# Performance work log

Hardware: AMD Instinct MI355X
Metric: run time of the kernel (lower is better)

Reference implementation:

```python
import jax, jax.numpy as jnp
import numpy as np

N_NODES = 100000
N_FEAT = 128
HID = 8
HEADS1 = 8
OUT2 = 32
NEG_SLOPE = 0.2


def gat_conv(x, W, a_src, a_dst, b, src, dst, n_nodes, concat):
    # x: [N, Fin], W: [Fin, H*C], a_src/a_dst: [H, C], b: [H*C] or [C]
    H, C = a_src.shape
    h = (x @ W).reshape(n_nodes, H, C)                      # [N, H, C]
    e_src = jnp.sum(h * a_src, axis=-1)                     # [N, H]
    e_dst = jnp.sum(h * a_dst, axis=-1)                     # [N, H]
    e = jax.nn.leaky_relu(e_src[src] + e_dst[dst], NEG_SLOPE)  # [E, H]
    m = jax.ops.segment_max(e, dst, num_segments=n_nodes)   # [N, H] (self-loops => no empty segment)
    ex = jnp.exp(e - m[dst])                                # [E, H]
    denom = jax.ops.segment_sum(ex, dst, num_segments=n_nodes)
    alpha = ex / denom[dst]                                 # [E, H]
    out = jax.ops.segment_sum(alpha[:, :, None] * h[src], dst, num_segments=n_nodes)  # [N, H, C]
    out = out.reshape(n_nodes, H * C) if concat else out.mean(axis=1)
    return out + b


def setup_inputs() -> dict:
    key = jax.random.key(0)
    ks = jax.random.split(key, 12)
    x = jax.random.normal(ks[0], (N_NODES, N_FEAT), dtype=jnp.float32)
    edge_index = jax.random.randint(ks[1], (2, 3200000), 0, N_NODES, dtype=jnp.int64)
    s1 = 1.0 / np.sqrt(N_FEAT)
    s2 = 1.0 / np.sqrt(HID * HEADS1)
    return {
        "x": x,
        "edge_index": edge_index,
        "W1": jax.random.normal(ks[2], (N_FEAT, HEADS1 * HID), dtype=jnp.float32) * s1,
        "a_src1": jax.random.normal(ks[3], (HEADS1, HID), dtype=jnp.float32) * s2,
        "a_dst1": jax.random.normal(ks[4], (HEADS1, HID), dtype=jnp.float32) * s2,
        "b1": jnp.zeros((HEADS1 * HID,), dtype=jnp.float32),
        "W2": jax.random.normal(ks[5], (HEADS1 * HID, OUT2), dtype=jnp.float32) * s2,
        "a_src2": jax.random.normal(ks[6], (1, OUT2), dtype=jnp.float32) * (1.0 / np.sqrt(OUT2)),
        "a_dst2": jax.random.normal(ks[7], (1, OUT2), dtype=jnp.float32) * (1.0 / np.sqrt(OUT2)),
        "b2": jnp.zeros((OUT2,), dtype=jnp.float32),
        "Wr": jax.random.normal(ks[8], (OUT2, 1), dtype=jnp.float32) * (1.0 / np.sqrt(OUT2)),
        "br": jnp.zeros((1,), dtype=jnp.float32),
    }


def reference(x, edge_index, W1, a_src1, a_dst1, b1, W2, a_src2, a_dst2, b2, Wr, br):
    n = x.shape[0]
    # PyG GATConv default add_self_loops=True
    loops = jnp.arange(n, dtype=edge_index.dtype)
    src = jnp.concatenate([edge_index[0], loops])
    dst = jnp.concatenate([edge_index[1], loops])
    h = gat_conv(x, W1, a_src1, a_dst1, b1, src, dst, n, concat=True)   # [N, 64]
    h = jax.nn.elu(h)
    h = gat_conv(h, W2, a_src2, a_dst2, b2, src, dst, n, concat=False)  # [N, 32]
    pooled = jnp.sum(h, axis=0, keepdims=True)                          # SumAggregation -> [1, 32]
    return pooled @ Wr + br                                             # [1, 1]
```

## Files before the change

### kernel.cpp

```cpp
#include <hip/hip_runtime.h>
#include <math.h>

#define NEG_SLOPE 0.2f
#define FIN 128
#define H1 8
#define F1 64
#define F2 32

#define SHIFT 5
#define BW 32
#define CAPL 2048
#define CAP_G 1408
#define NBMAX 4096

#define SB_SHIFT 11
#define NSBMAX 64
#define P_CHUNK 2048
#define BPS 35
#define SBCAP (BPS * P_CHUNK)

typedef unsigned short ushort_t;
typedef unsigned int uint_t;

#define LO16(u) __uint_as_float((u) << 16)
#define HI16(u) __uint_as_float((u) & 0xffff0000u)

#define FOLDQ4(x) { x += __shfl_xor(x, 16, 64); x += __shfl_xor(x, 32, 64); }
#define FOLD64(x) { x += __shfl_xor(x, 1, 64); x += __shfl_xor(x, 2, 64); x += __shfl_xor(x, 4, 64); \
                    x += __shfl_xor(x, 8, 64); x += __shfl_xor(x, 16, 64); x += __shfl_xor(x, 32, 64); }

static __device__ __forceinline__ ushort_t f2bf(float f) {
    uint_t u = __float_as_uint(f);
    u = (u + 0x7FFFu + ((u >> 16) & 1u)) >> 16;
    return (ushort_t)u;
}
static __device__ __forceinline__ uint_t packAB(float e) {
    return (uint_t)f2bf(__expf(e)) | ((uint_t)f2bf(__expf(NEG_SLOPE * e)) << 16);
}

__global__ void gemm1_kernel(const float* __restrict__ x, const float* __restrict__ W1,
                             const float* __restrict__ a_src, const float* __restrict__ a_dst,
                             ushort_t* __restrict__ h1, uint_t* __restrict__ sp,
                             float* __restrict__ ed, int N) {
    __shared__ float xs[16][FIN];
    int tid = threadIdx.x;
    int n0 = blockIdx.x * 16;
    for (int i = tid; i < 16 * FIN; i += 256) {
        int nn = n0 + (i >> 7);
        xs[i >> 7][i & 127] = (nn < N) ? x[(size_t)nn * FIN + (i & 127)] : 0.f;
    }
    __syncthreads();
    int wv = tid >> 6, j = tid & 63;
    int nb = wv << 2;
    float a0 = 0.f, a1 = 0.f, a2 = 0.f, a3 = 0.f;
#pragma unroll 2
    for (int k = 0; k < FIN; k += 4) {
        float w0 = W1[(k + 0) * F1 + j];
        float w1 = W1[(k + 1) * F1 + j];
        float w2 = W1[(k + 2) * F1 + j];
        float w3 = W1[(k + 3) * F1 + j];
        float4 x0 = *(const float4*)&xs[nb + 0][k];
        float4 x1 = *(const float4*)&xs[nb + 1][k];
        float4 x2 = *(const float4*)&xs[nb + 2][k];
        float4 x3 = *(const float4*)&xs[nb + 3][k];
        a0 = fmaf(x0.x, w0, fmaf(x0.y, w1, fmaf(x0.z, w2, fmaf(x0.w, w3, a0))));
        a1 = fmaf(x1.x, w0, fmaf(x1.y, w1, fmaf(x1.z, w2, fmaf(x1.w, w3, a1))));
        a2 = fmaf(x2.x, w0, fmaf(x2.y, w1, fmaf(x2.z, w2, fmaf(x2.w, w3, a2))));
        a3 = fmaf(x3.x, w0, fmaf(x3.y, w1, fmaf(x3.z, w2, fmaf(x3.w, w3, a3))));
    }
    float as = a_src[j], ad = a_dst[j];
    float av[4] = {a0, a1, a2, a3};
#pragma unroll
    for (int t = 0; t < 4; ++t) {
        int n = n0 + nb + t;
        if (n >= N) break;
        h1[(size_t)n * F1 + j] = f2bf(av[t]);
        float vs = av[t] * as;
        float vd = av[t] * ad;
#pragma unroll
        for (int off = 4; off >= 1; off >>= 1) {
            vs += __shfl_down(vs, off, 8);
            vd += __shfl_down(vd, off, 8);
        }
        if ((j & 7) == 0) {
            sp[n * H1 + (j >> 3)] = packAB(vs);
            ed[n * H1 + (j >> 3)] = vd;
        }
    }
}

__global__ void zerob_kernel(int* __restrict__ bcnt, int* __restrict__ boff,
                             int NB, float* __restrict__ pooled, int capg,
                             int* __restrict__ sbcnt, int nsb) {
    int t = blockIdx.x * blockDim.x + threadIdx.x;
    int stride = gridDim.x * blockDim.x;
    for (int i = t; i < NB; i += stride) {
        bcnt[i] = 0;
        if (capg) boff[i] = i * capg;
    }
    for (int i = t; i < nsb; i += stride) sbcnt[i] = 0;
    if (t == 0) pooled[0] = 0.f;
}

__global__ void __launch_bounds__(256, 4)
part1_kernel(const int* __restrict__ ei, int E, int N,
             int* __restrict__ sbcnt, uint_t* __restrict__ sbdata) {
    __shared__ int hist[NSBMAX];
    __shared__ int loff[NSBMAX];
    __shared__ int lcur[NSBMAX];
    __shared__ int gb[NSBMAX];
    __shared__ uint_t buf[P_CHUNK];
    __shared__ unsigned char sbarr[P_CHUNK];
    int tid = threadIdx.x;
    int NSB = (N + ((1 << SB_SHIFT) - 1)) >> SB_SHIFT;
    for (int i = tid; i < NSB; i += 256) hist[i] = 0;
    __syncthreads();
    int EN = E + N;
    int base = blockIdx.x * P_CHUNK;
    int m = EN - base; if (m > P_CHUNK) m = P_CHUNK;
    int t0 = base + tid * 8;
    int s[8], d[8];
    bool fast = (t0 + 8 <= E) && ((E & 3) == 0);
    if (fast) {
        int4 a = *(const int4*)&ei[t0];
        int4 b = *(const int4*)&ei[t0 + 4];
        s[0]=a.x; s[1]=a.y; s[2]=a.z; s[3]=a.w; s[4]=b.x; s[5]=b.y; s[6]=b.z; s[7]=b.w;
        int4 c = *(const int4*)&ei[E + t0];
        int4 e2 = *(const int4*)&ei[E + t0 + 4];
        d[0]=c.x; d[1]=c.y; d[2]=c.z; d[3]=c.w; d[4]=e2.x; d[5]=e2.y; d[6]=e2.z; d[7]=e2.w;
    } else {
#pragma unroll
        for (int r = 0; r < 8; ++r) {
            int t = t0 + r;
            if (t < EN) {
                if (t < E) { s[r] = ei[t]; d[r] = ei[E + t]; }
                else       { s[r] = d[r] = t - E; }
            } else d[r] = -1;
        }
    }
#pragma unroll
    for (int r = 0; r < 8; ++r)
        if (d[r] >= 0) atomicAdd(&hist[d[r] >> SB_SHIFT], 1);
    __syncthreads();
    if (tid < 64) {
        int v = (tid < NSB) ? hist[tid] : 0;
        int e = v;
#pragma unroll
        for (int o = 1; o < 64; o <<= 1) {
            int u = __shfl_up(e, o, 64);
            if (tid >= o) e += u;
        }
        e -= v;
        if (tid < NSB) {
            loff[tid] = e;
            lcur[tid] = e;
            gb[tid] = v ? atomicAdd(&sbcnt[tid], v) : 0;
        }
    }
    __syncthreads();
#pragma unroll
    for (int r = 0; r < 8; ++r)
        if (d[r] >= 0) {
            int sb = d[r] >> SB_SHIFT;
            int pos = atomicAdd(&lcur[sb], 1);
            buf[pos] = ((uint_t)s[r] << SB_SHIFT) | (uint_t)(d[r] & ((1 << SB_SHIFT) - 1));
            sbarr[pos] = (unsigned char)sb;
        }
    __syncthreads();
    for (int i = tid; i < m; i += 256) {
        int sb = sbarr[i];
        int idx = gb[sb] + (i - loff[sb]);
        if (idx < SBCAP)
            sbdata[(size_t)sb * SBCAP + idx] = buf[i];
    }
}

__global__ void __launch_bounds__(256, 4)
part2_kernel(const uint_t* __restrict__ sbdata, const int* __restrict__ sbcnt,
             int* __restrict__ bcnt, const int* __restrict__ boff,
             uint_t* __restrict__ pk) {
    __shared__ int hist[64];
    __shared__ int loff[64];
    __shared__ int lcur[64];
    __shared__ int gb[64];
    __shared__ uint_t buf[P_CHUNK];
    int tid = threadIdx.x;
    int sb = blockIdx.x / BPS;
    int base = (blockIdx.x % BPS) * P_CHUNK;
    int cnt = sbcnt[sb];
    if (cnt > SBCAP) cnt = SBCAP;
    if (base >= cnt) return;
    int m = cnt - base; if (m > P_CHUNK) m = P_CHUNK;
    if (tid < 64) hist[tid] = 0;
    __syncthreads();
    const uint_t* src = sbdata + (size_t)sb * SBCAP + base;
    uint_t v[8];
#pragma unroll
    for (int r = 0; r < 8; ++r) {
        int i = tid + r * 256;
        if (i < m) {
            v[r] = src[i];
            atomicAdd(&hist[(v[r] >> 5) & 63], 1);
        }
    }
    __syncthreads();
    if (tid < 64) {
        int c = hist[tid];
        int e = c;
#pragma unroll
        for (int o = 1; o < 64; o <<= 1) {
            int u = __shfl_up(e, o, 64);
            if (tid >= o) e += u;
        }
        e -= c;
        loff[tid] = e;
        lcur[tid] = e;
        int bucket = (sb << 6) + tid;
        gb[tid] = c ? (boff[bucket] + atomicAdd(&bcnt[bucket], c)) : 0;
    }
    __syncthreads();
#pragma unroll
    for (int r = 0; r < 8; ++r) {
        int i = tid + r * 256;
        if (i < m) {
            int lb = (v[r] >> 5) & 63;
            int pos = atomicAdd(&lcur[lb], 1);
            buf[pos] = v[r];
        }
    }
    __syncthreads();
    for (int i = tid; i < m; i += 256) {
        uint_t u = buf[i];
        int lb = (u >> 5) & 63;
        int idx = gb[lb] + (i - loff[lb]);
        pk[idx] = ((u >> SB_SHIFT) << SHIFT) | (u & (BW - 1));
    }
}

__global__ void bhist_kernel(const int* __restrict__ ei, int E, int N,
                             int* __restrict__ bcnt, int NB) {
    __shared__ int h[NBMAX];
    int tid = threadIdx.x;
    for (int i = tid; i < NB; i += 256) h[i] = 0;
    __syncthreads();
    int EN = E + N;
    int chunk = (EN + gridDim.x - 1) / gridDim.x;
    int e0 = blockIdx.x * chunk;
    int e1 = e0 + chunk; if (e1 > EN) e1 = EN;
    for (int t = e0 + tid; t < e1; t += 256) {
        int d = (t < E) ? ei[E + t] : (t - E);
        atomicAdd(&h[d >> SHIFT], 1);
    }
    __syncthreads();
    for (int i = tid; i < NB; i += 256)
        if (h[i]) atomicAdd(&bcnt[i], h[i]);
}

__global__ void bscan_kernel(const int* __restrict__ bcnt, int NB,
                             int* __restrict__ boff, int* __restrict__ bcur) {
    int lane = threadIdx.x;
    int chunk = (NB + 63) >> 6;
    int lo = lane * chunk;
    int hi = lo + chunk; if (hi > NB) hi = NB;
    int sum = 0;
    for (int i = lo; i < hi; ++i) sum += bcnt[i];
    int e = sum;
#pragma unroll
    for (int o = 1; o < 64; o <<= 1) {
        int v = __shfl_up(e, o, 64);
        if (lane >= o) e += v;
    }
    e -= sum;
    int run = e;
    for (int i = lo; i < hi; ++i) {
        int c = bcnt[i];
        boff[i] = run;
        bcur[i] = run;
        run += c;
    }
}

__global__ void bscat_kernel(const int* __restrict__ ei, int E, int N,
                             int* __restrict__ bcur, uint_t* __restrict__ pk, int NB) {
    __shared__ int lh[NBMAX];
    __shared__ int lc[NBMAX];
    int tid = threadIdx.x;
    for (int i = tid; i < NB; i += 256) lh[i] = 0;
    __syncthreads();
    int EN = E + N;
    int chunk = (EN + gridDim.x - 1) / gridDim.x;
    int e0 = blockIdx.x * chunk;
    int e1 = e0 + chunk; if (e1 > EN) e1 = EN;
    for (int t = e0 + tid; t < e1; t += 256) {
        int d = (t < E) ? ei[E + t] : (t - E);
        atomicAdd(&lh[d >> SHIFT], 1);
    }
    __syncthreads();
    for (int i = tid; i < NB; i += 256) {
        int c = lh[i];
        lc[i] = c ? atomicAdd(&bcur[i], c) : 0;
    }
    __syncthreads();
    for (int t = e0 + tid; t < e1; t += 256) {
        int s, d;
        if (t < E) { s = ei[t]; d = ei[E + t]; } else { s = d = t - E; }
        int pos = atomicAdd(&lc[d >> SHIFT], 1);
        pk[pos] = ((uint_t)s << SHIFT) | (uint_t)(d & (BW - 1));
    }
}

__global__ void __launch_bounds__(256, 8)
edge1_fused(const int* __restrict__ bcnt, const int* __restrict__ boff,
            uint_t* __restrict__ pk,
            const uint_t* __restrict__ sp, const float* __restrict__ ed,
            const ushort_t* __restrict__ h1,
            const float* __restrict__ b1, const float* __restrict__ W2,
            const float* __restrict__ a_src2, const float* __restrict__ a_dst2,
            const float* __restrict__ Wr,
            uint2* __restrict__ rec, float* __restrict__ ed2,
            int* __restrict__ loffg, int* __restrict__ ldegg, int N) {
    int b = blockIdx.x;
    int d0 = b << SHIFT;
    int cnt = bcnt[b];
    int gbase = boff[b];
    int tid = threadIdx.x;
    int wv = tid >> 6;
    int L = tid & 63;
    int q = L >> 4;
    int c4 = (L & 15) << 2;
    int hL = (L & 15) >> 1;
    __shared__ int ldeg[BW], loff[BW], lcur[BW];
    __shared__ int lsrc[CAPL];
    __shared__ float a1s[BW][F1];
    if (cnt <= CAPL) {
        if (tid < BW) ldeg[tid] = 0;
        __syncthreads();
        for (int k = tid; k < cnt; k += 256) atomicAdd(&ldeg[pk[gbase + k] & (BW - 1)], 1);
        __syncthreads();
        if (tid < BW) {
            int v = ldeg[tid];
            int e = v;
#pragma unroll
            for (int o = 1; o < BW; o <<= 1) {
                int u = __shfl_up(e, o, 64);
                if (tid >= o) e += u;
            }
            e -= v;
            loff[tid] = e;
            lcur[tid] = e;
        }
        __syncthreads();
        for (int k = tid; k < cnt; k += 256) {
            uint_t v = pk[gbase + k];
            int pos = atomicAdd(&lcur[v & (BW - 1)], 1);
            lsrc[pos] = (int)(v >> SHIFT);
        }
        __syncthreads();
        for (int k = tid; k < cnt; k += 256) pk[gbase + k] = (uint_t)lsrc[k];
        if (tid < BW) {
            loffg[d0 + tid] = loff[tid];
            ldegg[d0 + tid] = ldeg[tid];
        }
        for (int ld = wv * 8; ld < wv * 8 + 8; ++ld) {
            int d = d0 + ld;
            if (d >= N) break;
            int st = loff[ld], en = st + ldeg[ld];
            float edv = ed[d * H1 + hL];
            float Ad = __expf(edv), Bd = __expf(NEG_SLOPE * edv);
            float ax = 0.f, ay = 0.f, az = 0.f, aw = 0.f, wsum = 0.f;
            uint_t U0, U1; uint2 V0, V1;
            {
                int i0 = st + q, i1 = st + 4 + q;
                bool ok0 = i0 < en, ok1 = i1 < en;
                int s0 = lsrc[ok0 ? i0 : st];
                int s1 = lsrc[ok1 ? i1 : st];
                uint_t u0 = sp[s0 * H1 + hL];
                uint_t u1 = sp[s1 * H1 + hL];
                V0 = *(const uint2*)(h1 + ((size_t)s0 << 6) + c4);
                V1 = *(const uint2*)(h1 + ((size_t)s1 << 6) + c4);
                U0 = ok0 ? u0 : 0u;
                U1 = ok1 ? u1 : 0u;
            }
            for (int k = st; k < en; k += 8) {
                uint_t N0, N1; uint2 P0, P1;
                {
                    int i0 = k + 8 + q, i1 = k + 12 + q;
                    bool ok0 = i0 < en, ok1 = i1 < en;
                    int s0 = lsrc[ok0 ? i0 : st];
                    int s1 = lsrc[ok1 ? i1 : st];
                    uint_t u0 = sp[s0 * H1 + hL];
                    uint_t u1 = sp[s1 * H1 + hL];
                    P0 = *(const uint2*)(h1 + ((size_t)s0 << 6) + c4);
                    P1 = *(const uint2*)(h1 + ((size_t)s1 << 6) + c4);
                    N0 = ok0 ? u0 : 0u;
                    N1 = ok1 ? u1 : 0u;
                }
                float w0 = fmaxf(LO16(U0) * Ad, HI16(U0) * Bd);
                float w1 = fmaxf(LO16(U1) * Ad, HI16(U1) * Bd);
                ax = fmaf(w0, LO16(V0.x), ax);
                ay = fmaf(w0, HI16(V0.x), ay);
                az = fmaf(w0, LO16(V0.y), az);
                aw = fmaf(w0, HI16(V0.y), aw);
                ax = fmaf(w1, LO16(V1.x), ax);
                ay = fmaf(w1, HI16(V1.x), ay);
                az = fmaf(w1, LO16(V1.y), az);
                aw = fmaf(w1, HI16(V1.y), aw);
                wsum += w0 + w1;
                U0 = N0; U1 = N1; V0 = P0; V1 = P1;
            }
            FOLDQ4(ax); FOLDQ4(ay); FOLDQ4(az); FOLDQ4(aw); FOLDQ4(wsum);
            if (q == 0) {
                float inv = 1.f / wsum;
                a1s[ld][c4 + 0] = ax * inv;
                a1s[ld][c4 + 1] = ay * inv;
                a1s[ld][c4 + 2] = az * inv;
                a1s[ld][c4 + 3] = aw * inv;
            }
        }
    } else {
        for (int ld = wv * 8; ld < wv * 8 + 8; ++ld) {
            int d = d0 + ld;
            if (d >= N) break;
            float edv = ed[d * H1 + hL];
            float Ad = __expf(edv), Bd = __expf(NEG_SLOPE * edv);
            float ax = 0.f, ay = 0.f, az = 0.f, aw = 0.f, wsum = 0.f;
            for (int k0 = 0; k0 < cnt; k0 += 4) {
                int idx = k0 + q;
                bool ok = idx < cnt;
                uint_t v = pk[gbase + (ok ? idx : 0)];
                int s = (int)(v >> SHIFT);
                bool m = ok && ((int)(v & (BW - 1)) == ld);
                uint_t u = sp[(uint_t)s * H1 + hL];
                float w = m ? fmaxf(LO16(u) * Ad, HI16(u) * Bd) : 0.f;
                uint2 hv = *(const uint2*)(h1 + ((size_t)s << 6) + c4);
                ax = fmaf(w, LO16(hv.x), ax);
                ay = fmaf(w, HI16(hv.x), ay);
                az = fmaf(w, LO16(hv.y), az);
                aw = fmaf(w, HI16(hv.y), aw);
                wsum += w;
            }
            FOLDQ4(ax); FOLDQ4(ay); FOLDQ4(az); FOLDQ4(aw); FOLDQ4(wsum);
            if (q == 0) {
                float inv = 1.f / wsum;
                a1s[ld][c4 + 0] = ax * inv;
                a1s[ld][c4 + 1] = ay * inv;
                a1s[ld][c4 + 2] = az * inv;
                a1s[ld][c4 + 3] = aw * inv;
            }
        }
    }
    int nd = N - d0; if (nd > BW) nd = BW;
    __syncthreads();
    for (int i = tid; i < BW * F1; i += 256) {
        int dd = i >> 6;
        if (dd < nd) {
            int k = i & 63;
            float v = a1s[dd][k] + b1[k];
            a1s[dd][k] = v > 0.f ? v : expm1f(v);
        }
    }
    __syncthreads();
    int half = tid >> 5, j = tid & 31;
#pragma unroll
    for (int pass = 0; pass < 4; ++pass) {
        int ld2 = half + (pass << 3);
        if (ld2 < nd) {
            float acc = 0.f;
#pragma unroll
            for (int k = 0; k < F1; ++k) acc = fmaf(a1s[ld2][k], W2[k * F2 + j], acc);
            float vs = acc * a_src2[j];
            float vd = acc * a_dst2[j];
            float vg = acc * Wr[j];
#pragma unroll
            for (int off = 16; off >= 1; off >>= 1) {
                vs += __shfl_down(vs, off, 32);
                vd += __shfl_down(vd, off, 32);
                vg += __shfl_down(vg, off, 32);
            }
            if (j == 0) {
                int d = d0 + ld2;
                uint2 r; r.x = packAB(vs); r.y = __float_as_uint(vg);
                rec[d] = r;
                ed2[d] = vd;
            }
        }
    }
}

__global__ void __launch_bounds__(256, 8)
edge2_gather(const int* __restrict__ bcnt, const int* __restrict__ boff,
             const uint_t* __restrict__ pk,
             const int* __restrict__ loffg, const int* __restrict__ ldegg,
             const uint2* __restrict__ rec, const float* __restrict__ ed2,
             const float* __restrict__ b2, const float* __restrict__ Wr,
             float* __restrict__ pooled, int N) {
    int b = blockIdx.x;
    int d0 = b << SHIFT;
    int cnt = bcnt[b];
    int gbase = boff[b];
    int tid = threadIdx.x;
    int wv = tid >> 6;
    int L = tid & 63;
    __shared__ float ls[4];
    float t0 = (L < F2) ? b2[L] * Wr[L] : 0.f;
    FOLD64(t0);
    float b2w = t0;
    float part = 0.f;
    if (cnt <= CAPL) {
        for (int ld = wv * 8; ld < wv * 8 + 8; ++ld) {
            int d = d0 + ld;
            if (d >= N) break;
            int st = gbase + loffg[d];
            int dg = ldegg[d];
            float edv = ed2[d];
            float Ad = __expf(edv), Bd = __expf(NEG_SLOPE * edv);
            float acc = 0.f, wsm = 0.f;
            for (int k = 0; k < dg; k += 64) {
                int i = k + L;
                bool ok = i < dg;
                int s = (int)pk[st + (ok ? i : 0)];
                uint2 r = rec[s];
                float w = ok ? fmaxf(LO16(r.x) * Ad, HI16(r.x) * Bd) : 0.f;
                acc = fmaf(w, __uint_as_float(r.y), acc);
                wsm += w;
            }
            FOLD64(acc); FOLD64(wsm);
            part += acc / wsm + b2w;
        }
    } else {
        for (int ld = wv * 8; ld < wv * 8 + 8; ++ld) {
            int d = d0 + ld;
            if (d >= N) break;
            float edv = ed2[d];
            float Ad = __expf(edv), Bd = __expf(NEG_SLOPE * edv);
            float acc = 0.f, wsm = 0.f;
            for (int k0 = 0; k0 < cnt; k0 += 64) {
                int i = k0 + L;
                bool ok = i < cnt;
                uint_t v = pk[gbase + (ok ? i : 0)];
                int s = (int)(v >> SHIFT);
                bool mm = ok && ((int)(v & (BW - 1)) == ld);
                uint2 r = rec[s];
                float w = mm ? fmaxf(LO16(r.x) * Ad, HI16(r.x) * Bd) : 0.f;
                acc = fmaf(w, __uint_as_float(r.y), acc);
                wsm += w;
            }
            FOLD64(acc); FOLD64(wsm);
            part += acc / wsm + b2w;
        }
    }
    if (L == 0) ls[wv] = part;
    __syncthreads();
    if (tid == 0) atomicAdd(pooled, ls[0] + ls[1] + ls[2] + ls[3]);
}

__global__ void final_kernel(const float* __restrict__ pooled, const float* __restrict__ br,
                             float* __restrict__ out) {
    if (threadIdx.x == 0 && blockIdx.x == 0) out[0] = pooled[0] + br[0];
}

static inline size_t al128(size_t v) { return (v + 127) & ~(size_t)127; }

extern "C" void kernel_launch(void* const* d_in, const int* in_sizes, int n_in,
                              void* d_out, int out_size, void* d_ws, size_t ws_size,
                              hipStream_t stream) {
    const float* x    = (const float*)d_in[0];
    const int*   ei   = (const int*)d_in[1];
    const float* W1   = (const float*)d_in[2];
    const float* a_s1 = (const float*)d_in[3];
    const float* a_d1 = (const float*)d_in[4];
    const float* b1   = (const float*)d_in[5];
    const float* W2   = (const float*)d_in[6];
    const float* a_s2 = (const float*)d_in[7];
    const float* a_d2 = (const float*)d_in[8];
    const float* b2   = (const float*)d_in[9];
    const float* Wr   = (const float*)d_in[10];
    const float* br   = (const float*)d_in[11];
    float* out = (float*)d_out;

    int N = in_sizes[0] / FIN;
    int E = in_sizes[1] / 2;
    size_t n = (size_t)N;
    int NB = (N + BW - 1) >> SHIFT;
    int NSB = (N + ((1 << SB_SHIFT) - 1)) >> SB_SHIFT;

    char* ws = (char*)d_ws;
    size_t off_scr = 0;
    size_t off_sp1 = al128(off_scr + n * 256);
    size_t off_ed1 = al128(off_sp1 + n * 32 + 32);
    size_t off_h1  = al128(off_ed1 + n * 32);
    size_t off_pk  = al128(off_h1 + n * 128 + 128);
    uint_t*   sp1  = (uint_t*)(ws + off_sp1);
    float*    ed1  = (float*)(ws + off_ed1);
    ushort_t* h1   = (ushort_t*)(ws + off_h1);
    uint_t*   pk   = (uint_t*)(ws + off_pk);
    size_t pk_static = (size_t)NB * CAP_G * 4;
    size_t pk_exact  = (size_t)(E + N) * 4;
    uint_t* sbdata = (uint_t*)(ws + off_scr);
    size_t off_rec  = off_scr;
    size_t off_ed2  = al128(off_rec + (size_t)NB * BW * 8);
    size_t off_lofg = al128(off_ed2 + (size_t)NB * BW * 4);
    size_t off_ldgg = al128(off_lofg + (size_t)NB * BW * 4);
    uint2* rec   = (uint2*)(ws + off_rec);
    float* ed2   = (float*)(ws + off_ed2);
    int*   loffg = (int*)(ws + off_lofg);
    int*   ldegg = (int*)(ws + off_ldgg);
    bool use_static = (NSB <= NSBMAX) &&
                      ((size_t)NSB * SBCAP * 4 <= n * 256) &&
                      (off_ldgg + (size_t)NB * BW * 4 <= n * 256) &&
                      (ws_size >= off_pk + pk_static + (size_t)NBMAX * 16 +
                                  (size_t)NSBMAX * 4 + 128);
    char* tail = ws + off_pk + (use_static ? pk_static : pk_exact);
    int*      bcnt  = (int*)tail;
    int*      boff  = (int*)(tail + NBMAX * 4);
    int*      bcur  = (int*)(tail + NBMAX * 8);
    int*      sbcnt = (int*)(tail + NBMAX * 12);
    float*  pooled  = (float*)(tail + NBMAX * 12 + NSBMAX * 4);

    zerob_kernel<<<8, 256, 0, stream>>>(bcnt, boff, NB, pooled,
                                        use_static ? CAP_G : 0, sbcnt, NSB);
    if (use_static) {
        int EN = E + N;
        int G1 = (EN + P_CHUNK - 1) / P_CHUNK;
        part1_kernel<<<G1, 256, 0, stream>>>(ei, E, N, sbcnt, sbdata);
        part2_kernel<<<NSB * BPS, 256, 0, stream>>>(sbdata, sbcnt, bcnt, boff, pk);
        gemm1_kernel<<<(N + 15) / 16, 256, 0, stream>>>(x, W1, a_s1, a_d1, h1, sp1, ed1, N);
    } else {
        gemm1_kernel<<<(N + 15) / 16, 256, 0, stream>>>(x, W1, a_s1, a_d1, h1, sp1, ed1, N);
        bhist_kernel<<<256, 256, 0, stream>>>(ei, E, N, bcnt, NB);
        bscan_kernel<<<1, 64, 0, stream>>>(bcnt, NB, boff, bcur);
        bscat_kernel<<<256, 256, 0, stream>>>(ei, E, N, bcur, pk, NB);
    }
    edge1_fused<<<NB, 256, 0, stream>>>(bcnt, boff, pk, sp1, ed1, h1,
                                        b1, W2, a_s2, a_d2, Wr,
                                        rec, ed2, loffg, ldegg, N);
    edge2_gather<<<NB, 256, 0, stream>>>(bcnt, boff, pk, loffg, ldegg,
                                         rec, ed2, b2, Wr, pooled, N);
    final_kernel<<<1, 64, 0, stream>>>(pooled, br, out);
}
```

Baseline: 372.7 us.

## Use per-wavefront LDS histograms and vectorize the layer-2 projection

Shared-memory histogram and cursor counters in the two partition kernels and the layer-1 gather are split into four per-wavefront copies. Their offsets are derived from the combined prefix scan, which is meant to cut LDS atomic contention on hot buckets. The per-node 64x32 projection at the end of the layer-1 kernel is remapped so each thread computes 4 outputs with float4 loads from a padded shared array and then reduces across 8 lanes. This replaces the old scheme of 32 lanes each doing a full scalar dot product. The changes add LDS footprint and a slightly more complex scan, and the per-wave cursors change the order of edges within a bucket.

```diff
diff --git a/kernel.cpp b/kernel.cpp
--- a/kernel.cpp
+++ b/kernel.cpp
@@ -5,6 +5,7 @@
 #define FIN 128
 #define H1 8
 #define F1 64
+#define F1P 68
 #define F2 32
 
 #define SHIFT 5
@@ -105,15 +106,16 @@
 __global__ void __launch_bounds__(256, 4)
 part1_kernel(const int* __restrict__ ei, int E, int N,
              int* __restrict__ sbcnt, uint_t* __restrict__ sbdata) {
-    __shared__ int hist[NSBMAX];
+    __shared__ int histw[4][NSBMAX];
+    __shared__ int lcurw[4][NSBMAX];
     __shared__ int loff[NSBMAX];
-    __shared__ int lcur[NSBMAX];
     __shared__ int gb[NSBMAX];
     __shared__ uint_t buf[P_CHUNK];
     __shared__ unsigned char sbarr[P_CHUNK];
     int tid = threadIdx.x;
+    int wv = tid >> 6;
     int NSB = (N + ((1 << SB_SHIFT) - 1)) >> SB_SHIFT;
-    for (int i = tid; i < NSB; i += 256) hist[i] = 0;
+    for (int i = tid; i < 4 * NSBMAX; i += 256) ((int*)histw)[i] = 0;
     __syncthreads();
     int EN = E + N;
     int base = blockIdx.x * P_CHUNK;
@@ -140,21 +142,29 @@
     }
 #pragma unroll
     for (int r = 0; r < 8; ++r)
-        if (d[r] >= 0) atomicAdd(&hist[d[r] >> SB_SHIFT], 1);
+        if (d[r] >= 0) atomicAdd(&histw[wv][d[r] >> SB_SHIFT], 1);
     __syncthreads();
     if (tid < 64) {
-        int v = (tid < NSB) ? hist[tid] : 0;
-        int e = v;
+        int h0 = 0, h1 = 0, h2 = 0, h3 = 0;
+        if (tid < NSB) {
+            h0 = histw[0][tid]; h1 = histw[1][tid];
+            h2 = histw[2][tid]; h3 = histw[3][tid];
+        }
+        int tot = h0 + h1 + h2 + h3;
+        int e = tot;
 #pragma unroll
         for (int o = 1; o < 64; o <<= 1) {
             int u = __shfl_up(e, o, 64);
             if (tid >= o) e += u;
         }
-        e -= v;
+        e -= tot;
         if (tid < NSB) {
             loff[tid] = e;
-            lcur[tid] = e;
-            gb[tid] = v ? atomicAdd(&sbcnt[tid], v) : 0;
+            gb[tid] = tot ? atomicAdd(&sbcnt[tid], tot) : 0;
+            lcurw[0][tid] = e;
+            lcurw[1][tid] = e + h0;
+            lcurw[2][tid] = e + h0 + h1;
+            lcurw[3][tid] = e + h0 + h1 + h2;
         }
     }
     __syncthreads();
@@ -162,7 +172,7 @@
     for (int r = 0; r < 8; ++r)
         if (d[r] >= 0) {
             int sb = d[r] >> SB_SHIFT;
-            int pos = atomicAdd(&lcur[sb], 1);
+            int pos = atomicAdd(&lcurw[wv][sb], 1);
             buf[pos] = ((uint_t)s[r] << SB_SHIFT) | (uint_t)(d[r] & ((1 << SB_SHIFT) - 1));
             sbarr[pos] = (unsigned char)sb;
         }
@@ -179,19 +189,20 @@
 part2_kernel(const uint_t* __restrict__ sbdata, const int* __restrict__ sbcnt,
              int* __restrict__ bcnt, const int* __restrict__ boff,
              uint_t* __restrict__ pk) {
-    __shared__ int hist[64];
+    __shared__ int histw[4][64];
+    __shared__ int lcurw[4][64];
     __shared__ int loff[64];
-    __shared__ int lcur[64];
     __shared__ int gb[64];
     __shared__ uint_t buf[P_CHUNK];
     int tid = threadIdx.x;
+    int wv = tid >> 6;
     int sb = blockIdx.x / BPS;
     int base = (blockIdx.x % BPS) * P_CHUNK;
     int cnt = sbcnt[sb];
     if (cnt > SBCAP) cnt = SBCAP;
     if (base >= cnt) return;
     int m = cnt - base; if (m > P_CHUNK) m = P_CHUNK;
-    if (tid < 64) hist[tid] = 0;
+    for (int i = tid; i < 4 * 64; i += 256) ((int*)histw)[i] = 0;
     __syncthreads();
     const uint_t* src = sbdata + (size_t)sb * SBCAP + base;
     uint_t v[8];
@@ -200,23 +211,28 @@
         int i = tid + r * 256;
         if (i < m) {
             v[r] = src[i];
-            atomicAdd(&hist[(v[r] >> 5) & 63], 1);
+            atomicAdd(&histw[wv][(v[r] >> 5) & 63], 1);
         }
     }
     __syncthreads();
     if (tid < 64) {
-        int c = hist[tid];
-        int e = c;
+        int h0 = histw[0][tid], h1 = histw[1][tid];
+        int h2 = histw[2][tid], h3 = histw[3][tid];
+        int tot = h0 + h1 + h2 + h3;
+        int e = tot;
 #pragma unroll
         for (int o = 1; o < 64; o <<= 1) {
             int u = __shfl_up(e, o, 64);
             if (tid >= o) e += u;
         }
-        e -= c;
+        e -= tot;
         loff[tid] = e;
-        lcur[tid] = e;
         int bucket = (sb << 6) + tid;
-        gb[tid] = c ? (boff[bucket] + atomicAdd(&bcnt[bucket], c)) : 0;
+        gb[tid] = tot ? (boff[bucket] + atomicAdd(&bcnt[bucket], tot)) : 0;
+        lcurw[0][tid] = e;
+        lcurw[1][tid] = e + h0;
+        lcurw[2][tid] = e + h0 + h1;
+        lcurw[3][tid] = e + h0 + h1 + h2;
     }
     __syncthreads();
 #pragma unroll
@@ -224,7 +240,7 @@
         int i = tid + r * 256;
         if (i < m) {
             int lb = (v[r] >> 5) & 63;
-            int pos = atomicAdd(&lcur[lb], 1);
+            int pos = atomicAdd(&lcurw[wv][lb], 1);
             buf[pos] = v[r];
         }
     }
@@ -329,16 +345,20 @@
     int q = L >> 4;
     int c4 = (L & 15) << 2;
     int hL = (L & 15) >> 1;
-    __shared__ int ldeg[BW], loff[BW], lcur[BW];
+    __shared__ int ldeg[BW], loff[BW];
+    __shared__ int ldegw[4][BW], lcurw[4][BW];
     __shared__ int lsrc[CAPL];
-    __shared__ float a1s[BW][F1];
+    __shared__ float a1s[BW][F1P];
     if (cnt <= CAPL) {
-        if (tid < BW) ldeg[tid] = 0;
+        for (int i = tid; i < 4 * BW; i += 256) ((int*)ldegw)[i] = 0;
         __syncthreads();
-        for (int k = tid; k < cnt; k += 256) atomicAdd(&ldeg[pk[gbase + k] & (BW - 1)], 1);
+        for (int k = tid; k < cnt; k += 256)
+            atomicAdd(&ldegw[wv][pk[gbase + k] & (BW - 1)], 1);
         __syncthreads();
         if (tid < BW) {
-            int v = ldeg[tid];
+            int h0 = ldegw[0][tid], h1_ = ldegw[1][tid];
+            int h2 = ldegw[2][tid], h3 = ldegw[3][tid];
+            int v = h0 + h1_ + h2 + h3;
             int e = v;
 #pragma unroll
             for (int o = 1; o < BW; o <<= 1) {
@@ -347,12 +367,16 @@
             }
             e -= v;
             loff[tid] = e;
-            lcur[tid] = e;
+            ldeg[tid] = v;
+            lcurw[0][tid] = e;
+            lcurw[1][tid] = e + h0;
+            lcurw[2][tid] = e + h0 + h1_;
+            lcurw[3][tid] = e + h0 + h1_ + h2;
         }
         __syncthreads();
         for (int k = tid; k < cnt; k += 256) {
             uint_t v = pk[gbase + k];
-            int pos = atomicAdd(&lcur[v & (BW - 1)], 1);
+            int pos = atomicAdd(&lcurw[wv][v & (BW - 1)], 1);
             lsrc[pos] = (int)(v >> SHIFT);
         }
         __syncthreads();
@@ -460,29 +484,39 @@
         }
     }
     __syncthreads();
-    int half = tid >> 5, j = tid & 31;
-#pragma unroll
-    for (int pass = 0; pass < 4; ++pass) {
-        int ld2 = half + (pass << 3);
-        if (ld2 < nd) {
-            float acc = 0.f;
-#pragma unroll
-            for (int k = 0; k < F1; ++k) acc = fmaf(a1s[ld2][k], W2[k * F2 + j], acc);
-            float vs = acc * a_src2[j];
-            float vd = acc * a_dst2[j];
-            float vg = acc * Wr[j];
-#pragma unroll
-            for (int off = 16; off >= 1; off >>= 1) {
-                vs += __shfl_down(vs, off, 32);
-                vd += __shfl_down(vd, off, 32);
-                vg += __shfl_down(vg, off, 32);
-            }
-            if (j == 0) {
-                int d = d0 + ld2;
-                uint2 r; r.x = packAB(vs); r.y = __float_as_uint(vg);
-                rec[d] = r;
-                ed2[d] = vd;
-            }
+    int row = tid >> 3;
+    int jq = (tid & 7) << 2;
+    if (row < nd) {
+        float4 as2 = *(const float4*)&a_src2[jq];
+        float4 ad2 = *(const float4*)&a_dst2[jq];
+        float4 wr4 = *(const float4*)&Wr[jq];
+        float c0 = 0.f, c1 = 0.f, c2 = 0.f, c3 = 0.f;
+#pragma unroll
+        for (int k = 0; k < F1; k += 4) {
+            float4 a  = *(const float4*)&a1s[row][k];
+            float4 w0 = *(const float4*)&W2[(k + 0) * F2 + jq];
+            float4 w1 = *(const float4*)&W2[(k + 1) * F2 + jq];
+            float4 w2 = *(const float4*)&W2[(k + 2) * F2 + jq];
+            float4 w3 = *(const float4*)&W2[(k + 3) * F2 + jq];
+            c0 = fmaf(a.x, w0.x, fmaf(a.y, w1.x, fmaf(a.z, w2.x, fmaf(a.w, w3.x, c0))));
+            c1 = fmaf(a.x, w0.y, fmaf(a.y, w1.y, fmaf(a.z, w2.y, fmaf(a.w, w3.y, c1))));
+            c2 = fmaf(a.x, w0.z, fmaf(a.y, w1.z, fmaf(a.z, w2.z, fmaf(a.w, w3.z, c2))));
+            c3 = fmaf(a.x, w0.w, fmaf(a.y, w1.w, fmaf(a.z, w2.w, fmaf(a.w, w3.w, c3))));
+        }
+        float vs = c0 * as2.x + c1 * as2.y + c2 * as2.z + c3 * as2.w;
+        float vd = c0 * ad2.x + c1 * ad2.y + c2 * ad2.z + c3 * ad2.w;
+        float vg = c0 * wr4.x + c1 * wr4.y + c2 * wr4.z + c3 * wr4.w;
+#pragma unroll
+        for (int off = 4; off >= 1; off >>= 1) {
+            vs += __shfl_down(vs, off, 8);
+            vd += __shfl_down(vd, off, 8);
+            vg += __shfl_down(vg, off, 8);
+        }
+        if ((tid & 7) == 0) {
+            int d = d0 + row;
+            uint2 r; r.x = packAB(vs); r.y = __float_as_uint(vg);
+            rec[d] = r;
+            ed2[d] = vd;
         }
     }
 }
```

New measurement: 383.7 us. +2.9%, slower.
